# Optimization experiments

Measured on AMD Instinct MI355X. Metric: run time of the kernel, lower is better.

The kernel has to match this reference:

```python
import jax, jax.numpy as jnp
import numpy as np

N = 100000   # nodes
E = 1600000  # edges (avg degree 16)
D_IN = 128
H = 256
D_OUT = 128


def setup_inputs() -> dict:
    key = jax.random.key(0)
    ks = jax.random.split(key, 12)

    def lin_w(k, fan_in, fan_out):
        # torch nn.Linear-style uniform init
        bound = 1.0 / np.sqrt(fan_in)
        return jax.random.uniform(k, (fan_in, fan_out), jnp.float32, -bound, bound)

    return {
        "in_feat": jax.random.normal(ks[0], (N, D_IN), jnp.float32),
        "src": jax.random.randint(ks[1], (E,), 0, N, jnp.int32),
        "dst": jax.random.randint(ks[2], (E,), 0, N, jnp.int32),
        "Wc0": lin_w(ks[3], D_IN, H), "bc0": jnp.zeros((H,), jnp.float32),
        "Wc1": lin_w(ks[4], H, H),    "bc1": jnp.zeros((H,), jnp.float32),
        "Wc2": lin_w(ks[5], H, D_OUT),"bc2": jnp.zeros((D_OUT,), jnp.float32),
        "Wr0": lin_w(ks[6], D_OUT, H),"br0": jnp.zeros((H,), jnp.float32),
        "Wr1": lin_w(ks[7], H, H),    "br1": jnp.zeros((H,), jnp.float32),
        "Wr2": lin_w(ks[8], H, D_IN), "br2": jnp.zeros((D_IN,), jnp.float32),
    }


def _graph_conv(h, src, dst, W, b):
    """DGL GraphConv, norm='both': D_out^{-1/2} A D_in^{-1/2} h W + b."""
    ones = jnp.ones(src.shape[0], h.dtype)
    out_deg = jnp.clip(jax.ops.segment_sum(ones, src, num_segments=N), 1.0)
    in_deg = jnp.clip(jax.ops.segment_sum(ones, dst, num_segments=N), 1.0)
    h = h * (out_deg ** -0.5)[:, None]
    h = h @ W                                    # transform before aggregate
    h = jax.ops.segment_sum(h[src], dst, num_segments=N)  # SpMM aggregation
    return h * (in_deg ** -0.5)[:, None] + b


def reference(in_feat, src, dst, Wc0, bc0, Wc1, bc1, Wc2, bc2,
              Wr0, br0, Wr1, br1, Wr2, br2):
    h = jnp.tanh(_graph_conv(in_feat, src, dst, Wc0, bc0))
    h = jnp.tanh(_graph_conv(h, src, dst, Wc1, bc1))
    h = jax.nn.softmax(_graph_conv(h, src, dst, Wc2, bc2), axis=1)
    r = jnp.tanh(h @ Wr0 + br0)
    r = jnp.tanh(r @ Wr1 + br1)
    r = jax.nn.softmax(r @ Wr2 + br2, axis=1)
    return (h, r)
```

## Files before the change

kernel.cpp:

```cpp
#include <hip/hip_runtime.h>

typedef __attribute__((ext_vector_type(8))) short short8;
typedef __attribute__((ext_vector_type(4))) float f32x4;
typedef __attribute__((ext_vector_type(2))) float f32x2;

__device__ __forceinline__ ushort f2bf(float v) {
    unsigned u = __builtin_bit_cast(unsigned, v);
    unsigned r = (u + 0x7FFFu + ((u >> 16) & 1u)) >> 16;
    return (ushort)r;
}
__device__ __forceinline__ float lo16(unsigned p) { return __builtin_bit_cast(float, p << 16); }
__device__ __forceinline__ float hi16(unsigned p) { return __builtin_bit_cast(float, p & 0xFFFF0000u); }

__device__ __forceinline__ float fast_tanh(float x) {
    float cx = fminf(fmaxf(x, -9.f), 9.f);
    float e = __expf(2.f * cx);
    return (e - 1.f) / (e + 1.f);
}

__device__ __forceinline__ void async16(const void* g, void* l) {
    __builtin_amdgcn_global_load_lds(
        (const __attribute__((address_space(1))) unsigned*)g,
        (__attribute__((address_space(3))) unsigned*)l, 16, 0, 0);
}

#define BSHIFT 9
#define CCHUNK 2048

__global__ __launch_bounds__(256) void bucket_count(const int* __restrict__ src,
        const int* __restrict__ dst, int* __restrict__ gbc,
        int* __restrict__ outc, int E) {
    __shared__ int cnt[4][256];
    int t = threadIdx.x;
    int wv = t >> 6;
    ((int4*)cnt)[t] = make_int4(0, 0, 0, 0);
    __syncthreads();
    int start = blockIdx.x * CCHUNK;
#pragma unroll
    for (int k = 0; k < 2; ++k) {
        int i = start + (k * 256 + t) * 4;
        if (i + 3 < E) {
            int4 d = *(const int4*)(dst + i);
            int4 s = *(const int4*)(src + i);
            atomicAdd(&cnt[wv][d.x >> BSHIFT], 1);
            atomicAdd(&cnt[wv][d.y >> BSHIFT], 1);
            atomicAdd(&cnt[wv][d.z >> BSHIFT], 1);
            atomicAdd(&cnt[wv][d.w >> BSHIFT], 1);
            atomicAdd(&outc[s.x], 1);
            atomicAdd(&outc[s.y], 1);
            atomicAdd(&outc[s.z], 1);
            atomicAdd(&outc[s.w], 1);
        } else {
#pragma unroll
            for (int m = 0; m < 4; ++m) {
                int ii = i + m;
                if (ii < E) {
                    atomicAdd(&cnt[wv][dst[ii] >> BSHIFT], 1);
                    atomicAdd(&outc[src[ii]], 1);
                }
            }
        }
    }
    __syncthreads();
    int sum = cnt[0][t] + cnt[1][t] + cnt[2][t] + cnt[3][t];
    if (sum) atomicAdd(&gbc[t], sum);
}

__global__ void scan_buckets(const int* __restrict__ gbc, int* __restrict__ bucketBase,
                             int* __restrict__ pairCursor, int* __restrict__ roff,
                             int N, int E) {
    __shared__ int s[256];
    int t = threadIdx.x;
    int v = gbc[t];
    s[t] = v; __syncthreads();
    for (int o = 1; o < 256; o <<= 1) {
        int y = (t >= o) ? s[t - o] : 0;
        __syncthreads();
        s[t] += y;
        __syncthreads();
    }
    int excl = s[t] - v;
    bucketBase[t] = excl;
    pairCursor[t] = excl;
    if (t == 255) bucketBase[256] = s[255];
    if (t == 0) roff[N] = E;
}

__global__ __launch_bounds__(256) void part_scatter(const int* __restrict__ src,
        const int* __restrict__ dst, int* __restrict__ pairCursor,
        uint2* __restrict__ pairs, int E) {
    __shared__ int cnt[256];
    __shared__ int base[256];
    int t = threadIdx.x;
    cnt[t] = 0;
    __syncthreads();
    int start = blockIdx.x * CCHUNK;
    int dd[8], sv[8], bk[8], rk[8];
#pragma unroll
    for (int k = 0; k < 2; ++k) {
        int i = start + (k * 256 + t) * 4;
        if (i + 3 < E) {
            int4 d = *(const int4*)(dst + i);
            int4 s = *(const int4*)(src + i);
            dd[4 * k + 0] = d.x; dd[4 * k + 1] = d.y; dd[4 * k + 2] = d.z; dd[4 * k + 3] = d.w;
            sv[4 * k + 0] = s.x; sv[4 * k + 1] = s.y; sv[4 * k + 2] = s.z; sv[4 * k + 3] = s.w;
        } else {
#pragma unroll
            for (int m = 0; m < 4; ++m) {
                int ii = i + m;
                if (ii < E) { dd[4 * k + m] = dst[ii]; sv[4 * k + m] = src[ii]; }
                else        { dd[4 * k + m] = -1; sv[4 * k + m] = 0; }
            }
        }
    }
#pragma unroll
    for (int e = 0; e < 8; ++e) {
        if (dd[e] >= 0) {
            bk[e] = dd[e] >> BSHIFT;
            rk[e] = atomicAdd(&cnt[bk[e]], 1);
        } else bk[e] = -1;
    }
    __syncthreads();
    base[t] = cnt[t] ? atomicAdd(&pairCursor[t], cnt[t]) : 0;
    __syncthreads();
#pragma unroll
    for (int e = 0; e < 8; ++e)
        if (bk[e] >= 0) pairs[base[bk[e]] + rk[e]] = make_uint2((unsigned)sv[e], (unsigned)dd[e]);
}

__global__ __launch_bounds__(1024) void build_bucket(const uint2* __restrict__ pairs,
        const int* __restrict__ bucketBase, int* __restrict__ roff,
        float* __restrict__ sIn, int* __restrict__ csr, int N) {
    __shared__ int cnt[512];
    __shared__ int cur[512];
    __shared__ int ss[256];
    int b = blockIdx.x;
    int t = threadIdx.x;
    int lo = b << BSHIFT;
    int s0 = bucketBase[b], s1 = bucketBase[b + 1];
    if (t < 512) cnt[t] = 0;
    __syncthreads();
    for (int j = s0 + t; j < s1; j += 1024)
        atomicAdd(&cnt[pairs[j].y - lo], 1);
    __syncthreads();
    int c0 = 0, c1 = 0;
    if (t < 256) { c0 = cnt[2 * t]; c1 = cnt[2 * t + 1]; ss[t] = c0 + c1; }
    __syncthreads();
    for (int o = 1; o < 256; o <<= 1) {
        int y = 0;
        if (t < 256 && t >= o) y = ss[t - o];
        __syncthreads();
        if (t < 256) ss[t] += y;
        __syncthreads();
    }
    if (t < 256) {
        int eb = ss[t] - (c0 + c1);
        int p0 = s0 + eb, p1 = s0 + eb + c0;
        cur[2 * t] = p0; cur[2 * t + 1] = p1;
        int n0 = lo + 2 * t, n1 = n0 + 1;
        if (n0 < N) { roff[n0] = p0; sIn[n0] = rsqrtf((float)(c0 > 0 ? c0 : 1)); }
        if (n1 < N) { roff[n1] = p1; sIn[n1] = rsqrtf((float)(c1 > 0 ? c1 : 1)); }
    }
    __syncthreads();
    for (int j = s0 + t; j < s1; j += 1024) {
        uint2 p = pairs[j];
        int pos = atomicAdd(&cur[p.y - lo], 1);
        csr[pos] = (int)p.x;
    }
}

__global__ void convw(const float* w0, const float* w1, const float* w2,
                      const float* w3, const float* w4, const float* w5,
                      ushort* __restrict__ Wt) {
    int i = blockIdx.x * 256 + threadIdx.x;
    int base, Km, Nm; const float* W;
    if      (i < 32768)  { base = 0;      Km = 128; Nm = 256; W = w0; }
    else if (i < 98304)  { base = 32768;  Km = 256; Nm = 256; W = w1; }
    else if (i < 131072) { base = 98304;  Km = 256; Nm = 128; W = w2; }
    else if (i < 163840) { base = 131072; Km = 128; Nm = 256; W = w3; }
    else if (i < 229376) { base = 163840; Km = 256; Nm = 256; W = w4; }
    else                 { base = 229376; Km = 256; Nm = 128; W = w5; }
    int l = i - base;
    int k = l / Nm, n = l % Nm;
    Wt[base + n * Km + k] = f2bf(W[l]);
}

__global__ void prescale(const float* __restrict__ x, const int* __restrict__ outc,
                         ushort* __restrict__ o, float* __restrict__ sOut,
                         int total ) {
    int i = blockIdx.x * 256 + threadIdx.x;
    if (i >= total) return;
    int row = i >> 5;
    int oc = outc[row]; if (oc < 1) oc = 1;
    float s = rsqrtf((float)oc);
    if ((i & 31) == 0) sOut[row] = s;
    float4 v = ((const float4*)x)[i];
    ushort4 r;
    r.x = f2bf(v.x * s); r.y = f2bf(v.y * s);
    r.z = f2bf(v.z * s); r.w = f2bf(v.w * s);
    ((ushort4*)o)[i] = r;
}

__global__ __launch_bounds__(256) void agg128(const ushort* __restrict__ F,
        const int* __restrict__ csr, const int* __restrict__ roff,
        const float* __restrict__ sIn, ushort* __restrict__ out, int N) {
    int w = blockIdx.x * 4 + (threadIdx.x >> 6);
    if (w >= N) return;
    int lane = threadIdx.x & 63;
    int b = roff[w], e = roff[w + 1];
    int deg = e - b;
    int n = deg < 64 ? deg : 64;
    float a0 = 0.f, a1 = 0.f;
    const char* base = (const char*)(F + lane * 2);
    int voff = 0;
    if (n > 0) voff = csr[b + (lane < n ? lane : n - 1)] << 8;
    int j = 0;
    for (; j + 16 <= n; j += 16) {
        unsigned p[16];
#pragma unroll
        for (int k = 0; k < 16; ++k) {
            int o = __shfl(voff, j + k, 64);
            p[k] = *(const unsigned*)(base + (size_t)(unsigned)o);
        }
#pragma unroll
        for (int k = 0; k < 16; ++k) { a0 += lo16(p[k]); a1 += hi16(p[k]); }
    }
    for (; j + 8 <= n; j += 8) {
        unsigned p[8];
#pragma unroll
        for (int k = 0; k < 8; ++k) {
            int o = __shfl(voff, j + k, 64);
            p[k] = *(const unsigned*)(base + (size_t)(unsigned)o);
        }
#pragma unroll
        for (int k = 0; k < 8; ++k) { a0 += lo16(p[k]); a1 += hi16(p[k]); }
    }
    for (; j < n; ++j) {
        int o = __shfl(voff, j, 64);
        unsigned p = *(const unsigned*)(base + (size_t)(unsigned)o);
        a0 += lo16(p); a1 += hi16(p);
    }
    for (int i = b + 64; i < e; ++i) {
        unsigned p = *(const unsigned*)(base + ((size_t)csr[i] << 8));
        a0 += lo16(p); a1 += hi16(p);
    }
    float s = sIn[w];
    ushort2 o2; o2.x = f2bf(a0 * s); o2.y = f2bf(a1 * s);
    *(ushort2*)(out + (size_t)w * 128 + lane * 2) = o2;
}

__global__ __launch_bounds__(256) void agg256f8(const unsigned char* __restrict__ F,
        const int* __restrict__ csr, const int* __restrict__ roff,
        const float* __restrict__ sIn, ushort* __restrict__ out, int N) {
    int w = blockIdx.x * 4 + (threadIdx.x >> 6);
    if (w >= N) return;
    int lane = threadIdx.x & 63;
    int b = roff[w], e = roff[w + 1];
    int deg = e - b;
    int n = deg < 64 ? deg : 64;
    float a0 = 0.f, a1 = 0.f, a2 = 0.f, a3 = 0.f;
    const char* base = (const char*)F + lane * 4;
    int voff = 0;
    if (n > 0) voff = csr[b + (lane < n ? lane : n - 1)] << 8;
    int j = 0;
    for (; j + 16 <= n; j += 16) {
        unsigned p[16];
#pragma unroll
        for (int k = 0; k < 16; ++k) {
            int o = __shfl(voff, j + k, 64);
            p[k] = *(const unsigned*)(base + (size_t)(unsigned)o);
        }
#pragma unroll
        for (int k = 0; k < 16; ++k) {
            f32x2 lo = __builtin_amdgcn_cvt_pk_f32_fp8(p[k], false);
            f32x2 hi = __builtin_amdgcn_cvt_pk_f32_fp8(p[k], true);
            a0 += lo.x; a1 += lo.y; a2 += hi.x; a3 += hi.y;
        }
    }
    for (; j + 8 <= n; j += 8) {
        unsigned p[8];
#pragma unroll
        for (int k = 0; k < 8; ++k) {
            int o = __shfl(voff, j + k, 64);
            p[k] = *(const unsigned*)(base + (size_t)(unsigned)o);
        }
#pragma unroll
        for (int k = 0; k < 8; ++k) {
            f32x2 lo = __builtin_amdgcn_cvt_pk_f32_fp8(p[k], false);
            f32x2 hi = __builtin_amdgcn_cvt_pk_f32_fp8(p[k], true);
            a0 += lo.x; a1 += lo.y; a2 += hi.x; a3 += hi.y;
        }
    }
    for (; j < n; ++j) {
        int o = __shfl(voff, j, 64);
        unsigned p = *(const unsigned*)(base + (size_t)(unsigned)o);
        f32x2 lo = __builtin_amdgcn_cvt_pk_f32_fp8(p, false);
        f32x2 hi = __builtin_amdgcn_cvt_pk_f32_fp8(p, true);
        a0 += lo.x; a1 += lo.y; a2 += hi.x; a3 += hi.y;
    }
    for (int i = b + 64; i < e; ++i) {
        unsigned p = *(const unsigned*)(base + ((size_t)csr[i] << 8));
        f32x2 lo = __builtin_amdgcn_cvt_pk_f32_fp8(p, false);
        f32x2 hi = __builtin_amdgcn_cvt_pk_f32_fp8(p, true);
        a0 += lo.x; a1 += lo.y; a2 += hi.x; a3 += hi.y;
    }
    float s = sIn[w];
    ushort4 o4;
    o4.x = f2bf(a0 * s); o4.y = f2bf(a1 * s);
    o4.z = f2bf(a2 * s); o4.w = f2bf(a3 * s);
    *(ushort4*)(out + (size_t)w * 256 + lane * 4) = o4;
}

__global__ __launch_bounds__(256) void agg_softmax(const ushort* __restrict__ F,
        const int* __restrict__ csr, const int* __restrict__ roff,
        const float* __restrict__ sIn, const float* __restrict__ bias,
        float* __restrict__ outh, ushort* __restrict__ outb, int N) {
    int w = blockIdx.x * 4 + (threadIdx.x >> 6);
    if (w >= N) return;
    int lane = threadIdx.x & 63;
    int b = roff[w], e = roff[w + 1];
    int deg = e - b;
    int n = deg < 64 ? deg : 64;
    float a0 = 0.f, a1 = 0.f;
    const char* base = (const char*)(F + lane * 2);
    int voff = 0;
    if (n > 0) voff = csr[b + (lane < n ? lane : n - 1)] << 8;
    int j = 0;
    for (; j + 16 <= n; j += 16) {
        unsigned p[16];
#pragma unroll
        for (int k = 0; k < 16; ++k) {
            int o = __shfl(voff, j + k, 64);
            p[k] = *(const unsigned*)(base + (size_t)(unsigned)o);
        }
#pragma unroll
        for (int k = 0; k < 16; ++k) { a0 += lo16(p[k]); a1 += hi16(p[k]); }
    }
    for (; j + 8 <= n; j += 8) {
        unsigned p[8];
#pragma unroll
        for (int k = 0; k < 8; ++k) {
            int o = __shfl(voff, j + k, 64);
            p[k] = *(const unsigned*)(base + (size_t)(unsigned)o);
        }
#pragma unroll
        for (int k = 0; k < 8; ++k) { a0 += lo16(p[k]); a1 += hi16(p[k]); }
    }
    for (; j < n; ++j) {
        int o = __shfl(voff, j, 64);
        unsigned p = *(const unsigned*)(base + (size_t)(unsigned)o);
        a0 += lo16(p); a1 += hi16(p);
    }
    for (int i = b + 64; i < e; ++i) {
        unsigned p = *(const unsigned*)(base + ((size_t)csr[i] << 8));
        a0 += lo16(p); a1 += hi16(p);
    }
    float s = sIn[w];
    float2 bb = *(const float2*)(bias + lane * 2);
    float l0 = a0 * s + bb.x, l1 = a1 * s + bb.y;
    float m = fmaxf(l0, l1);
    for (int o = 32; o; o >>= 1) m = fmaxf(m, __shfl_xor(m, o, 64));
    float e0 = __expf(l0 - m), e1 = __expf(l1 - m);
    float sm = e0 + e1;
    for (int o = 32; o; o >>= 1) sm += __shfl_xor(sm, o, 64);
    float inv = 1.f / sm;
    float r0 = e0 * inv, r1 = e1 * inv;
    float2 fo; fo.x = r0; fo.y = r1;
    *(float2*)(outh + (size_t)w * 128 + lane * 2) = fo;
    ushort2 o2; o2.x = f2bf(r0); o2.y = f2bf(r1);
    *(ushort2*)(outb + (size_t)w * 128 + lane * 2) = o2;
}

template <int MODE, int K>
__global__ __launch_bounds__(256) void gemm2(
        const ushort* __restrict__ A, const ushort* __restrict__ Wt,
        const float* __restrict__ bias, const float* __restrict__ rowscale,
        void* __restrict__ out, int M, int Nn) {
    constexpr int SLOTS = K / 8;
    constexpr int KS = K / 32;
    constexpr int RPI = 1024 / (2 * K);
    __shared__ ushort ldsW[128 * K];

    const int tid = threadIdx.x;
    const int lane = tid & 63;
    const int wid = tid >> 6;
    const int nby = Nn >> 7;
    const int bx = (int)blockIdx.x / nby;
    const int by = (int)blockIdx.x - bx * nby;
    const int rowbase = bx * 128;
    const int colbase = by * 128;

#pragma unroll
    for (int it = 0; it < 128 / (4 * RPI); ++it) {
        int row0 = it * (4 * RPI) + wid * RPI;
        int rl = row0 + lane / SLOTS;
        int sl = lane % SLOTS;
        int gs = sl ^ (rl & 7);
        async16(Wt + (size_t)(colbase + rl) * K + gs * 8,
                (char*)ldsW + row0 * (2 * K));
    }

    const int l15 = lane & 15, l4 = lane >> 4;
    short8 a[2][KS];
#pragma unroll
    for (int rt = 0; rt < 2; ++rt) {
        int grow = rowbase + wid * 32 + rt * 16 + l15;
        if (grow > M - 1) grow = M - 1;
        const ushort* ap = A + (size_t)grow * K + l4 * 8;
#pragma unroll
        for (int ks = 0; ks < KS; ++ks)
            a[rt][ks] = *(const short8*)(ap + ks * 32);
    }

    f32x4 acc[2][8];
#pragma unroll
    for (int i = 0; i < 2; ++i)
#pragma unroll
        for (int j = 0; j < 8; ++j) acc[i][j] = (f32x4){0.f, 0.f, 0.f, 0.f};

    __syncthreads();

#pragma unroll
    for (int ks = 0; ks < KS; ++ks) {
        short8 b[8];
#pragma unroll
        for (int ct = 0; ct < 8; ++ct) {
            int n = ct * 16 + l15;
            int slot = (ks * 4 + l4) ^ (n & 7);
            b[ct] = *(const short8*)&ldsW[n * K + slot * 8];
        }
#pragma unroll
        for (int ct = 0; ct < 8; ++ct) {
            acc[0][ct] = __builtin_amdgcn_mfma_f32_16x16x32_bf16(a[0][ks], b[ct], acc[0][ct], 0, 0, 0);
            acc[1][ct] = __builtin_amdgcn_mfma_f32_16x16x32_bf16(a[1][ks], b[ct], acc[1][ct], 0, 0, 0);
        }
    }

    float bv[8];
#pragma unroll
    for (int ct = 0; ct < 8; ++ct)
        bv[ct] = (MODE != 1 && bias) ? bias[colbase + ct * 16 + l15] : 0.f;

    if (MODE == 4) {
#pragma unroll
        for (int rt = 0; rt < 2; ++rt) {
#pragma unroll
            for (int rg = 0; rg < 4; ++rg) {
                int row = rowbase + wid * 32 + rt * 16 + l4 * 4 + rg;
                if (row >= M) continue;
                float sc = rowscale ? rowscale[row] : 1.f;
#pragma unroll
                for (int ct = 0; ct < 8; ++ct) {
                    float v = fast_tanh(acc[rt][ct][rg] + bv[ct]) * sc;
                    float vp = __shfl_xor(v, 1, 64);
                    if ((l15 & 1) == 0) {
                        int pk = __builtin_amdgcn_cvt_pk_fp8_f32(v, vp, 0, false);
                        *(ushort*)((char*)out + (size_t)row * Nn + colbase + ct * 16 + l15)
                            = (ushort)(pk & 0xFFFF);
                    }
                }
            }
        }
    } else if (MODE != 3) {
#pragma unroll
        for (int rt = 0; rt < 2; ++rt) {
#pragma unroll
            for (int rg = 0; rg < 4; ++rg) {
                int row = rowbase + wid * 32 + rt * 16 + l4 * 4 + rg;
                if (row >= M) continue;
                float sc = 1.f;
                if (MODE == 0 && rowscale) sc = rowscale[row];
#pragma unroll
                for (int ct = 0; ct < 8; ++ct) {
                    int col = colbase + ct * 16 + l15;
                    float v = acc[rt][ct][rg] + bv[ct];
                    if (MODE == 0) v = fast_tanh(v) * sc;
                    ((ushort*)out)[(size_t)row * Nn + col] = f2bf(v);
                }
            }
        }
    } else {
#pragma unroll
        for (int rt = 0; rt < 2; ++rt) {
#pragma unroll
            for (int rg = 0; rg < 4; ++rg) {
                int row = rowbase + wid * 32 + rt * 16 + l4 * 4 + rg;
                float m = acc[rt][0][rg] + bv[0];
#pragma unroll
                for (int ct = 1; ct < 8; ++ct) m = fmaxf(m, acc[rt][ct][rg] + bv[ct]);
                m = fmaxf(m, __shfl_xor(m, 1, 64));
                m = fmaxf(m, __shfl_xor(m, 2, 64));
                m = fmaxf(m, __shfl_xor(m, 4, 64));
                m = fmaxf(m, __shfl_xor(m, 8, 64));
                float ev[8], s = 0.f;
#pragma unroll
                for (int ct = 0; ct < 8; ++ct) {
                    ev[ct] = __expf(acc[rt][ct][rg] + bv[ct] - m);
                    s += ev[ct];
                }
                s += __shfl_xor(s, 1, 64);
                s += __shfl_xor(s, 2, 64);
                s += __shfl_xor(s, 4, 64);
                s += __shfl_xor(s, 8, 64);
                float inv = 1.f / s;
                if (row < M) {
#pragma unroll
                    for (int ct = 0; ct < 8; ++ct) {
                        int col = colbase + ct * 16 + l15;
                        ((float*)out)[(size_t)row * Nn + col] = ev[ct] * inv;
                    }
                }
            }
        }
    }
}

extern "C" void kernel_launch(void* const* d_in, const int* in_sizes, int n_in,
                              void* d_out, int out_size, void* d_ws, size_t ws_size,
                              hipStream_t stream) {
    (void)n_in; (void)out_size; (void)ws_size;
    const float* in_feat = (const float*)d_in[0];
    const int*   src     = (const int*)d_in[1];
    const int*   dstp    = (const int*)d_in[2];
    const float* Wc0 = (const float*)d_in[3];  const float* bc0 = (const float*)d_in[4];
    const float* Wc1 = (const float*)d_in[5];  const float* bc1 = (const float*)d_in[6];
    const float* Wc2 = (const float*)d_in[7];  const float* bc2 = (const float*)d_in[8];
    const float* Wr0 = (const float*)d_in[9];  const float* br0 = (const float*)d_in[10];
    const float* Wr1 = (const float*)d_in[11]; const float* br1 = (const float*)d_in[12];
    const float* Wr2 = (const float*)d_in[13]; const float* br2 = (const float*)d_in[14];

    const int N = in_sizes[0] / 128;
    const int E = in_sizes[1];
    const int numBuckets = (N + ((1 << BSHIFT) - 1)) >> BSHIFT;

    char* ws = (char*)d_ws;
    size_t off = 0;
    auto alloc = [&](size_t bytes) -> char* {
        char* p = ws + off;
        off += (bytes + 255) & ~(size_t)255;
        return p;
    };
    char* S1 = alloc((size_t)N * 256 * 2);
    char* S2 = alloc((size_t)N * 256 * 2);
    int* csr    = (int*)alloc((size_t)E * 4);
    int* roff   = (int*)alloc((size_t)(N + 1) * 4);
    int* outc   = (int*)alloc((size_t)N * 4);
    float* sOut = (float*)alloc((size_t)N * 4);
    float* sIn  = (float*)alloc((size_t)N * 4);
    ushort* Wt  = (ushort*)alloc(262144 * 2);
    int* gbc        = (int*)alloc(256 * 4);
    int* bucketBase = (int*)alloc(257 * 4);
    int* pairCursor = (int*)alloc(256 * 4);
    uint2* pairs = (uint2*)S2;

    hipMemsetAsync(outc, 0, (size_t)N * 4, stream);
    hipMemsetAsync(gbc, 0, 256 * 4, stream);

    int nblk = (E + CCHUNK - 1) / CCHUNK;
    bucket_count<<<nblk, 256, 0, stream>>>(src, dstp, gbc, outc, E);
    scan_buckets<<<1, 256, 0, stream>>>(gbc, bucketBase, pairCursor, roff, N, E);
    part_scatter<<<nblk, 256, 0, stream>>>(src, dstp, pairCursor, pairs, E);
    build_bucket<<<numBuckets, 1024, 0, stream>>>(pairs, bucketBase, roff, sIn, csr, N);

    convw<<<262144 / 256, 256, 0, stream>>>(Wc0, Wc1, Wc2, Wr0, Wr1, Wr2, Wt);

    ushort* Xs = (ushort*)S1;
    prescale<<<(N * 32 + 255) / 256, 256, 0, stream>>>(in_feat, outc, Xs, sOut, N * 32);

    int aggGrid = (N + 3) / 4;
    int nrb = (N + 127) / 128;

    ushort* A0 = (ushort*)S2;
    agg128<<<aggGrid, 256, 0, stream>>>(Xs, csr, roff, sIn, A0, N);
    unsigned char* B1f8 = (unsigned char*)S1;
    gemm2<4, 128><<<nrb * 2, 256, 0, stream>>>(A0, Wt, bc0, sOut, B1f8, N, 256);
    ushort* A1 = (ushort*)S2;
    agg256f8<<<aggGrid, 256, 0, stream>>>(B1f8, csr, roff, sIn, A1, N);
    ushort* B2 = (ushort*)S1;
    gemm2<0, 256><<<nrb * 2, 256, 0, stream>>>(A1, Wt + 32768, bc1, sOut, B2, N, 256);
    ushort* T3 = (ushort*)S2;
    gemm2<1, 256><<<nrb, 256, 0, stream>>>(B2, Wt + 98304, nullptr, nullptr, T3, N, 128);
    float* outh = (float*)d_out;
    ushort* Hbf = (ushort*)S1;
    agg_softmax<<<aggGrid, 256, 0, stream>>>(T3, csr, roff, sIn, bc2, outh, Hbf, N);
    ushort* R1 = (ushort*)S2;
    gemm2<0, 128><<<nrb * 2, 256, 0, stream>>>(Hbf, Wt + 131072, br0, nullptr, R1, N, 256);
    ushort* R2 = (ushort*)S1;
    gemm2<0, 256><<<nrb * 2, 256, 0, stream>>>(R1, Wt + 163840, br1, nullptr, R2, N, 256);
    gemm2<3, 256><<<nrb, 256, 0, stream>>>(R2, Wt + 229376, br2, nullptr,
                                           outh + (size_t)N * 128, N, 128);
}
```

Before: 710.8 us.

## Replace global out-degree atomics with bucketed source partition and per-bucket LDS counting

Out-degree counting previously used 1.6M global atomics on a per-node array. The new code bins source ids into 512-node buckets using LDS counters, scatters them into a bucketed buffer, then counts per bucket in shared memory in a new src_count kernel that writes the rsqrt scale directly. This removes the random global atomics and the outc memset. In exchange it adds an extra E-sized scatter write and read, plus a second scan and another kernel launch.

New measurement: 665.3 us. 1.07x faster.

```diff
diff --git a/kernel.cpp b/kernel.cpp
--- a/kernel.cpp
+++ b/kernel.cpp
@@ -28,12 +28,13 @@
 #define CCHUNK 2048
 
 __global__ __launch_bounds__(256) void bucket_count(const int* __restrict__ src,
-        const int* __restrict__ dst, int* __restrict__ gbc,
-        int* __restrict__ outc, int E) {
-    __shared__ int cnt[4][256];
+        const int* __restrict__ dst, int* __restrict__ gbc , int E) {
+    __shared__ int cd[4][256];
+    __shared__ int cs[4][256];
     int t = threadIdx.x;
     int wv = t >> 6;
-    ((int4*)cnt)[t] = make_int4(0, 0, 0, 0);
+    ((int4*)cd)[t] = make_int4(0, 0, 0, 0);
+    ((int4*)cs)[t] = make_int4(0, 0, 0, 0);
     __syncthreads();
     int start = blockIdx.x * CCHUNK;
 #pragma unroll
@@ -42,32 +43,35 @@
         if (i + 3 < E) {
             int4 d = *(const int4*)(dst + i);
             int4 s = *(const int4*)(src + i);
-            atomicAdd(&cnt[wv][d.x >> BSHIFT], 1);
-            atomicAdd(&cnt[wv][d.y >> BSHIFT], 1);
-            atomicAdd(&cnt[wv][d.z >> BSHIFT], 1);
-            atomicAdd(&cnt[wv][d.w >> BSHIFT], 1);
-            atomicAdd(&outc[s.x], 1);
-            atomicAdd(&outc[s.y], 1);
-            atomicAdd(&outc[s.z], 1);
-            atomicAdd(&outc[s.w], 1);
+            atomicAdd(&cd[wv][d.x >> BSHIFT], 1);
+            atomicAdd(&cd[wv][d.y >> BSHIFT], 1);
+            atomicAdd(&cd[wv][d.z >> BSHIFT], 1);
+            atomicAdd(&cd[wv][d.w >> BSHIFT], 1);
+            atomicAdd(&cs[wv][s.x >> BSHIFT], 1);
+            atomicAdd(&cs[wv][s.y >> BSHIFT], 1);
+            atomicAdd(&cs[wv][s.z >> BSHIFT], 1);
+            atomicAdd(&cs[wv][s.w >> BSHIFT], 1);
         } else {
 #pragma unroll
             for (int m = 0; m < 4; ++m) {
                 int ii = i + m;
                 if (ii < E) {
-                    atomicAdd(&cnt[wv][dst[ii] >> BSHIFT], 1);
-                    atomicAdd(&outc[src[ii]], 1);
+                    atomicAdd(&cd[wv][dst[ii] >> BSHIFT], 1);
+                    atomicAdd(&cs[wv][src[ii] >> BSHIFT], 1);
                 }
             }
         }
     }
     __syncthreads();
-    int sum = cnt[0][t] + cnt[1][t] + cnt[2][t] + cnt[3][t];
-    if (sum) atomicAdd(&gbc[t], sum);
+    int sd = cd[0][t] + cd[1][t] + cd[2][t] + cd[3][t];
+    int ssum = cs[0][t] + cs[1][t] + cs[2][t] + cs[3][t];
+    if (sd) atomicAdd(&gbc[t], sd);
+    if (ssum) atomicAdd(&gbc[256 + t], ssum);
 }
 
 __global__ void scan_buckets(const int* __restrict__ gbc, int* __restrict__ bucketBase,
-                             int* __restrict__ pairCursor, int* __restrict__ roff,
+                             int* __restrict__ pairCursor, int* __restrict__ srcBase,
+                             int* __restrict__ srcCursor, int* __restrict__ roff,
                              int N, int E) {
     __shared__ int s[256];
     int t = threadIdx.x;
@@ -79,23 +83,35 @@
         s[t] += y;
         __syncthreads();
     }
-    int excl = s[t] - v;
-    bucketBase[t] = excl;
-    pairCursor[t] = excl;
+    bucketBase[t] = s[t] - v;
+    pairCursor[t] = s[t] - v;
     if (t == 255) bucketBase[256] = s[255];
+    __syncthreads();
+    int v2 = gbc[256 + t];
+    s[t] = v2; __syncthreads();
+    for (int o = 1; o < 256; o <<= 1) {
+        int y = (t >= o) ? s[t - o] : 0;
+        __syncthreads();
+        s[t] += y;
+        __syncthreads();
+    }
+    srcBase[t] = s[t] - v2;
+    srcCursor[t] = s[t] - v2;
+    if (t == 255) srcBase[256] = s[255];
     if (t == 0) roff[N] = E;
 }
 
 __global__ __launch_bounds__(256) void part_scatter(const int* __restrict__ src,
         const int* __restrict__ dst, int* __restrict__ pairCursor,
-        uint2* __restrict__ pairs, int E) {
-    __shared__ int cnt[256];
-    __shared__ int base[256];
+        int* __restrict__ srcCursor, uint2* __restrict__ pairs,
+        int* __restrict__ sbuf, int E) {
+    __shared__ int cntd[256], based[256];
+    __shared__ int cnts[256], bases[256];
     int t = threadIdx.x;
-    cnt[t] = 0;
+    cntd[t] = 0; cnts[t] = 0;
     __syncthreads();
     int start = blockIdx.x * CCHUNK;
-    int dd[8], sv[8], bk[8], rk[8];
+    int dd[8], sv[8], rkd[8], rks[8];
 #pragma unroll
     for (int k = 0; k < 2; ++k) {
         int i = start + (k * 256 + t) * 4;
@@ -116,16 +132,38 @@
 #pragma unroll
     for (int e = 0; e < 8; ++e) {
         if (dd[e] >= 0) {
-            bk[e] = dd[e] >> BSHIFT;
-            rk[e] = atomicAdd(&cnt[bk[e]], 1);
-        } else bk[e] = -1;
-    }
-    __syncthreads();
-    base[t] = cnt[t] ? atomicAdd(&pairCursor[t], cnt[t]) : 0;
-    __syncthreads();
-#pragma unroll
-    for (int e = 0; e < 8; ++e)
-        if (bk[e] >= 0) pairs[base[bk[e]] + rk[e]] = make_uint2((unsigned)sv[e], (unsigned)dd[e]);
+            rkd[e] = atomicAdd(&cntd[dd[e] >> BSHIFT], 1);
+            rks[e] = atomicAdd(&cnts[sv[e] >> BSHIFT], 1);
+        }
+    }
+    __syncthreads();
+    based[t] = cntd[t] ? atomicAdd(&pairCursor[t], cntd[t]) : 0;
+    bases[t] = cnts[t] ? atomicAdd(&srcCursor[t], cnts[t]) : 0;
+    __syncthreads();
+#pragma unroll
+    for (int e = 0; e < 8; ++e) {
+        if (dd[e] >= 0) {
+            pairs[based[dd[e] >> BSHIFT] + rkd[e]] = make_uint2((unsigned)sv[e], (unsigned)dd[e]);
+            sbuf[bases[sv[e] >> BSHIFT] + rks[e]] = sv[e];
+        }
+    }
+}
+
+__global__ __launch_bounds__(256) void src_count(const int* __restrict__ sbuf,
+        const int* __restrict__ srcBase, float* __restrict__ sOut, int N) {
+    __shared__ int cnt[512];
+    int b = blockIdx.x;
+    int t = threadIdx.x;
+    int lo = b << BSHIFT;
+    int s0 = srcBase[b], s1 = srcBase[b + 1];
+    cnt[t] = 0; cnt[t + 256] = 0;
+    __syncthreads();
+    for (int j = s0 + t; j < s1; j += 256)
+        atomicAdd(&cnt[sbuf[j] - lo], 1);
+    __syncthreads();
+    int n0 = lo + 2 * t, n1 = n0 + 1;
+    if (n0 < N) { int c = cnt[2 * t];     sOut[n0] = rsqrtf((float)(c > 0 ? c : 1)); }
+    if (n1 < N) { int c = cnt[2 * t + 1]; sOut[n1] = rsqrtf((float)(c > 0 ? c : 1)); }
 }
 
 __global__ __launch_bounds__(1024) void build_bucket(const uint2* __restrict__ pairs,
@@ -185,15 +223,12 @@
     Wt[base + n * Km + k] = f2bf(W[l]);
 }
 
-__global__ void prescale(const float* __restrict__ x, const int* __restrict__ outc,
-                         ushort* __restrict__ o, float* __restrict__ sOut,
-                         int total ) {
+__global__ void prescale(const float* __restrict__ x, const float* __restrict__ sOut,
+                         ushort* __restrict__ o, int total ) {
     int i = blockIdx.x * 256 + threadIdx.x;
     if (i >= total) return;
     int row = i >> 5;
-    int oc = outc[row]; if (oc < 1) oc = 1;
-    float s = rsqrtf((float)oc);
-    if ((i & 31) == 0) sOut[row] = s;
+    float s = sOut[row];
     float4 v = ((const float4*)x)[i];
     ushort4 r;
     r.x = f2bf(v.x * s); r.y = f2bf(v.y * s);
@@ -544,28 +579,31 @@
     char* S2 = alloc((size_t)N * 256 * 2);
     int* csr    = (int*)alloc((size_t)E * 4);
     int* roff   = (int*)alloc((size_t)(N + 1) * 4);
-    int* outc   = (int*)alloc((size_t)N * 4);
+    int* sbuf   = (int*)alloc((size_t)E * 4);
     float* sOut = (float*)alloc((size_t)N * 4);
     float* sIn  = (float*)alloc((size_t)N * 4);
     ushort* Wt  = (ushort*)alloc(262144 * 2);
-    int* gbc        = (int*)alloc(256 * 4);
+    int* gbc        = (int*)alloc(512 * 4);
     int* bucketBase = (int*)alloc(257 * 4);
     int* pairCursor = (int*)alloc(256 * 4);
+    int* srcBase    = (int*)alloc(257 * 4);
+    int* srcCursor  = (int*)alloc(256 * 4);
     uint2* pairs = (uint2*)S2;
 
-    hipMemsetAsync(outc, 0, (size_t)N * 4, stream);
-    hipMemsetAsync(gbc, 0, 256 * 4, stream);
+    hipMemsetAsync(gbc, 0, 512 * 4, stream);
 
     int nblk = (E + CCHUNK - 1) / CCHUNK;
-    bucket_count<<<nblk, 256, 0, stream>>>(src, dstp, gbc, outc, E);
-    scan_buckets<<<1, 256, 0, stream>>>(gbc, bucketBase, pairCursor, roff, N, E);
-    part_scatter<<<nblk, 256, 0, stream>>>(src, dstp, pairCursor, pairs, E);
+    bucket_count<<<nblk, 256, 0, stream>>>(src, dstp, gbc, E);
+    scan_buckets<<<1, 256, 0, stream>>>(gbc, bucketBase, pairCursor, srcBase, srcCursor,
+                                        roff, N, E);
+    part_scatter<<<nblk, 256, 0, stream>>>(src, dstp, pairCursor, srcCursor, pairs, sbuf, E);
     build_bucket<<<numBuckets, 1024, 0, stream>>>(pairs, bucketBase, roff, sIn, csr, N);
+    src_count<<<numBuckets, 256, 0, stream>>>(sbuf, srcBase, sOut, N);
 
     convw<<<262144 / 256, 256, 0, stream>>>(Wc0, Wc1, Wc2, Wr0, Wr1, Wr2, Wt);
 
     ushort* Xs = (ushort*)S1;
-    prescale<<<(N * 32 + 255) / 256, 256, 0, stream>>>(in_feat, outc, Xs, sOut, N * 32);
+    prescale<<<(N * 32 + 255) / 256, 256, 0, stream>>>(in_feat, sOut, Xs, N * 32);
 
     int aggGrid = (N + 3) / 4;
     int nrb = (N + 127) / 128;
```
